# Performance work log

Hardware: AMD Instinct MI355X
Metric: run time of the kernel (lower is better)

## Reference

```python
import jax, jax.numpy as jnp
import numpy as np

B, D, L = 8, 512, 4096
NHEAD = 8
HEAD_DIM = D // NHEAD
TRUNC_STD = 0.02


def setup_inputs() -> dict:
    key = jax.random.key(0)
    ks = jax.random.split(key, 7)
    return {
        "x": jax.random.normal(ks[0], (B, D, L, 1), jnp.float32),
        "y": jax.random.normal(ks[1], (B, D, 1, 1), jnp.float32),
        "Wq": jax.random.normal(ks[2], (D, D), jnp.float32) * TRUNC_STD,
        "Wk": jax.random.normal(ks[3], (D, D), jnp.float32) * TRUNC_STD,
        "Wv": jax.random.normal(ks[4], (D, D), jnp.float32) * TRUNC_STD,
        "WO_ring": jax.random.normal(ks[5], (D, D), jnp.float32) * TRUNC_STD,
        "bO_ring": jnp.zeros((D,), jnp.float32),
        "WO_star": jax.random.normal(ks[6], (D, D), jnp.float32) * TRUNC_STD,
        "bO_star": jnp.zeros((D,), jnp.float32),
    }


def reference(x, y, Wq, Wk, Wv, WO_ring, bO_ring, WO_star, bO_star):
    Bx, Dx, Lx, _ = x.shape
    hd = Dx // NHEAD
    scale = 1.0 / np.sqrt(hd).astype(np.float32)

    # concat relay token on the sequence axis, project q/k/v over channels
    xy = jnp.concatenate([x, y], axis=2)[..., 0]            # [B, D, L+1]
    xy = jnp.transpose(xy, (0, 2, 1))                       # [B, L+1, D]
    q = jnp.transpose(xy @ Wq, (0, 2, 1))                   # [B, D, L+1]
    k = jnp.transpose(xy @ Wk, (0, 2, 1))
    v = jnp.transpose(xy @ Wv, (0, 2, 1))

    # ---- ring (local window-3 + relay) attention over the L node tokens ----
    qn = q[:, :, :Lx].reshape(Bx, NHEAD, hd, Lx)            # [B,n,h,L]
    kn, vn = k[:, :, :Lx], v[:, :, :Lx]                     # [B,D,L]
    kr, vr = k[:, :, Lx], v[:, :, Lx]                       # [B,D]

    def window3(t):
        # extract_patches SAME with size 3: slot w holds t[:, :, l-1+w], zero-padded
        tp = jnp.pad(t, ((0, 0), (0, 0), (1, 1)))
        tw = jnp.stack([tp[:, :, w:w + Lx] for w in range(3)], axis=2)  # [B,D,3,L]
        return tw.reshape(Bx, NHEAD, hd, 3, Lx)

    kr_b = jnp.broadcast_to(kr.reshape(Bx, NHEAD, hd, 1, 1), (Bx, NHEAD, hd, 1, Lx))
    vr_b = jnp.broadcast_to(vr.reshape(Bx, NHEAD, hd, 1, 1), (Bx, NHEAD, hd, 1, Lx))
    kw = jnp.concatenate([window3(kn), kr_b], axis=3)       # [B,n,h,4,L]
    vw = jnp.concatenate([window3(vn), vr_b], axis=3)

    scores = jnp.einsum('bnhl,bnhwl->bnwl', qn, kw) * scale  # [B,n,4,L]
    alphas = jax.nn.softmax(scores, axis=2)                  # softmax over window
    att = jnp.einsum('bnwl,bnhwl->bnhl', alphas, vw).reshape(Bx, Dx, Lx)
    nodes = jnp.einsum('bdl,de->bel', att, WO_ring) + bO_ring[None, :, None]
    nodes = nodes[..., None]                                 # [B, D, L, 1]

    # ---- star (relay) attention: relay query attends to all L+1 tokens ----
    qr = q[:, :, Lx].reshape(Bx, NHEAD, 1, hd)              # [B,n,1,h]
    ka = k.reshape(Bx, NHEAD, hd, Lx + 1)                   # [B,n,h,L+1]
    va = v.reshape(Bx, NHEAD, hd, Lx + 1)
    s = jnp.einsum('bnoh,bnhl->bnol', qr, ka) * scale       # [B,n,1,L+1]
    a = jax.nn.softmax(s, axis=-1)
    att_r = jnp.einsum('bnol,bnhl->bnoh', a, va).reshape(Bx, Dx)
    relay = (att_r @ WO_star + bO_star).reshape(Bx, Dx, 1, 1)

    return nodes, relay
```

## Files before the change

### kernel.cpp

```cpp
#include <hip/hip_runtime.h>

#define BB 8
#define DD 512
#define LL 4096
#define NH 8
#define HD 64
#define SCALE 0.125f
#define NCH2 128

typedef __attribute__((ext_vector_type(8))) short short8;
typedef __attribute__((ext_vector_type(4))) float f32x4;

static __device__ __forceinline__ float bf2f(unsigned short u) {
  union { float f; unsigned int i; } c; c.i = ((unsigned int)u) << 16; return c.f;
}
static __device__ __forceinline__ unsigned short f2bf(float f) {
  union { float f; unsigned int i; } c; c.f = f;
  unsigned int i = c.i;
  unsigned int r = (i + 0x7fffu + ((i >> 16) & 1u)) >> 16;
  return (unsigned short)r;
}

static __device__ __forceinline__ void gload_lds16(const void* g, void* l) {
  __builtin_amdgcn_global_load_lds(
      (const __attribute__((address_space(1))) void*)g,
      (__attribute__((address_space(3))) void*)l, 16, 0, 0);
}

static __device__ __forceinline__ float waveSum(float v) {
#pragma unroll
  for (int o = 32; o; o >>= 1) v += __shfl_down(v, o, 64);
  return v;
}
static __device__ __forceinline__ float grp8Sum(float v) {
  v += __shfl_xor(v, 1, 8);
  v += __shfl_xor(v, 2, 8);
  v += __shfl_xor(v, 4, 8);
  return v;
}
static __device__ __forceinline__ float waveAllMax(float v) {
#pragma unroll
  for (int o = 1; o < 64; o <<= 1) v = fmaxf(v, __shfl_xor(v, o, 64));
  return v;
}
static __device__ __forceinline__ float waveAllSum(float v) {
#pragma unroll
  for (int o = 1; o < 64; o <<= 1) v += __shfl_xor(v, o, 64);
  return v;
}

__global__ __launch_bounds__(256) void prep_w4(
    const float* __restrict__ w0, const float* __restrict__ w1,
    const float* __restrict__ w2, const float* __restrict__ w3,
    unsigned short* __restrict__ o0, unsigned short* __restrict__ o1,
    unsigned short* __restrict__ o2, unsigned short* __restrict__ o3) {
  const int s = blockIdx.z;
  const float* win = (s == 0) ? w0 : (s == 1) ? w1 : (s == 2) ? w2 : w3;
  unsigned short* wout = (s == 0) ? o0 : (s == 1) ? o1 : (s == 2) ? o2 : o3;
  const int d0 = blockIdx.y * 64;
  const int m0 = blockIdx.x * 64;
  __shared__ float t[64][65];
  const int tid = threadIdx.x;
  const int r = tid >> 4;
  const int c4 = (tid & 15) * 4;
#pragma unroll
  for (int p = 0; p < 4; p++) {
    const float4 v = *(const float4*)(win + (size_t)(d0 + p * 16 + r) * DD + m0 + c4);
    *(float4*)&t[p * 16 + r][c4] = v;
  }
  __syncthreads();
#pragma unroll
  for (int p = 0; p < 4; p++) {
    const int ll = p * 16 + r;
    ushort4 o;
    o.x = f2bf(t[c4 + 0][ll]);
    o.y = f2bf(t[c4 + 1][ll]);
    o.z = f2bf(t[c4 + 2][ll]);
    o.w = f2bf(t[c4 + 3][ll]);
    *(ushort4*)(wout + (size_t)(m0 + ll) * DD + d0 + c4) = o;
  }
}

__global__ __launch_bounds__(256) void prep_x(
    const float* __restrict__ x, unsigned short* __restrict__ xt) {
  const int b = blockIdx.z;
  const int e0 = blockIdx.y * 64;
  const int l0 = blockIdx.x * 64;
  __shared__ float t[64][65];
  const int tid = threadIdx.x;
  const int r = tid >> 4;
  const int c4 = (tid & 15) * 4;
  const float* xb = x + (size_t)b * DD * LL;
#pragma unroll
  for (int p = 0; p < 4; p++) {
    const float4 v = *(const float4*)(xb + (size_t)(e0 + p * 16 + r) * LL + l0 + c4);
    *(float4*)&t[p * 16 + r][c4] = v;
  }
  __syncthreads();
#pragma unroll
  for (int p = 0; p < 4; p++) {
    const int ll = p * 16 + r;
    ushort4 o;
    o.x = f2bf(t[c4 + 0][ll]);
    o.y = f2bf(t[c4 + 1][ll]);
    o.z = f2bf(t[c4 + 2][ll]);
    o.w = f2bf(t[c4 + 3][ll]);
    *(ushort4*)(xt + ((size_t)b * LL + l0 + ll) * DD + e0 + c4) = o;
  }
}

#define STAGEH(g, s)                                       \
  do {                                                     \
    gload_lds16((g) + sgoff, (s) + sloff);                 \
    gload_lds16((g) + sgoff + 32, (s) + sloff + 4096);     \
  } while (0)

#define READ_A(dst, base, ib)                                           \
  _Pragma("unroll") for (int i = 0; i < 4; i++) {                       \
    dst[i][0] = *(const short8*)((base) + ((ib) + i) * 512);            \
    dst[i][1] = *(const short8*)((base) + ((ib) + i) * 512 + 4096);     \
  }

#define READ_B(base, qn_)                                               \
  _Pragma("unroll") for (int j = 0; j < 2; j++) {                       \
    bb[j][0] = *(const short8*)((base) + (qn_) * 1024 + j * 512);       \
    bb[j][1] = *(const short8*)((base) + (qn_) * 1024 + j * 512 + 4096);\
  }

#define MFMA16(AF, IO, JO)                                                    \
  __builtin_amdgcn_s_setprio(1);                                              \
  _Pragma("unroll") for (int i = 0; i < 4; i++)                               \
  _Pragma("unroll") for (int j = 0; j < 2; j++) {                             \
    acc[(IO) + i][(JO) + j] = __builtin_amdgcn_mfma_f32_16x16x32_bf16(        \
        AF[i][0], bb[j][0], acc[(IO) + i][(JO) + j], 0, 0, 0);                \
    acc[(IO) + i][(JO) + j] = __builtin_amdgcn_mfma_f32_16x16x32_bf16(        \
        AF[i][1], bb[j][1], acc[(IO) + i][(JO) + j], 0, 0, 0);                \
  }                                                                           \
  __builtin_amdgcn_s_setprio(0);

#define PHASE_SYNC_PRE                                     \
  __builtin_amdgcn_s_barrier();                            \
  asm volatile("s_waitcnt lgkmcnt(0)" ::: "memory");       \
  __builtin_amdgcn_sched_barrier(0);

#define PHASE_SYNC_POST                                    \
  __builtin_amdgcn_sched_barrier(0);                       \
  __builtin_amdgcn_s_barrier();

__global__ __launch_bounds__(512, 2) void qkv_mfma_8ph(
    const unsigned short* __restrict__ Wt, const unsigned short* __restrict__ Xt,
    unsigned short* __restrict__ qn, unsigned short* __restrict__ kn,
    unsigned short* __restrict__ vn) {
  extern __shared__ __align__(16) unsigned short sm[];
  const int b = blockIdx.z;
  const int m0 = blockIdx.y * 256;
  const int n0 = blockIdx.x * 256;
  const int tid = threadIdx.x;
  const int lane = tid & 63, w = tid >> 6;
  const int wm = w >> 2, wn = w & 3;
  const int l15 = lane & 15, lh = lane >> 4;

  const unsigned short* Ag = Wt + (size_t)m0 * DD;
  const unsigned short* Bg = Xt + ((size_t)b * LL + n0) * DD;

  const int kswz = (lh << 3) ^ ((l15 & 8) << 1);
  const unsigned short* aB = sm + wm * 8192 + l15 * 32 + kswz;
  const unsigned short* bB = sm + 32768 + (wn >> 1) * 8192 + (wn & 1) * 2048 +
                             l15 * 32 + kswz;

  const int srow = (w << 4) + (lane >> 2);
  const size_t sgoff = (size_t)srow * DD + ((size_t)(((lane & 3) << 3) ^ ((srow & 8) << 1)));
  const int sloff = w * 512;

  f32x4 acc[8][4];
#pragma unroll
  for (int i = 0; i < 8; i++)
#pragma unroll
    for (int j = 0; j < 4; j++) acc[i][j] = (f32x4){0.f, 0.f, 0.f, 0.f};

  STAGEH(Ag, sm);
  STAGEH(Ag + 128 * DD, sm + 8192);
  STAGEH(Bg, sm + 32768);
  STAGEH(Bg + 128 * DD, sm + 32768 + 8192);
  STAGEH(Ag + 64, sm + 16384);
  STAGEH(Ag + 128 * DD + 64, sm + 16384 + 8192);
  asm volatile("s_waitcnt vmcnt(4)" ::: "memory");
  __builtin_amdgcn_s_barrier();

  short8 a0[4][2], a1[4][2], bb[2][2];
  for (int u = 0; u < 8; ++u) {
    const int slot = u & 1;
    const unsigned short* aS = aB + slot * 16384;
    const unsigned short* bS = bB + slot * 16384;
    const unsigned short* An = Ag + (u + 2) * 64;
    const unsigned short* Bn = Bg + (u + 1) * 64;
    unsigned short* sAd = sm + slot * 16384;
    unsigned short* sBd = sm + 32768 + (slot ^ 1) * 16384;

    READ_A(a0, aS, 0);
    READ_B(bS, 0);
    if (u < 7) STAGEH(Bn, sBd);
    PHASE_SYNC_PRE
    MFMA16(a0, 0, 0)
    PHASE_SYNC_POST
    READ_A(a1, aS, 4);
    if (u < 7) STAGEH(Bn + 128 * DD, sBd + 8192);
    PHASE_SYNC_PRE
    MFMA16(a1, 4, 0)
    PHASE_SYNC_POST
    READ_B(bS, 1);
    if (u < 6) STAGEH(An, sAd);
    PHASE_SYNC_PRE
    MFMA16(a0, 0, 2)
    PHASE_SYNC_POST
    if (u < 6) STAGEH(An + 128 * DD, sAd + 8192);
    __builtin_amdgcn_s_barrier();
    asm volatile("s_waitcnt lgkmcnt(0)" ::: "memory");
    __builtin_amdgcn_sched_barrier(0);
    MFMA16(a1, 4, 2)
    __builtin_amdgcn_sched_barrier(0);
    if (u < 6) {
      asm volatile("s_waitcnt vmcnt(4)" ::: "memory");
    } else if (u == 6) {
      asm volatile("s_waitcnt vmcnt(0)" ::: "memory");
    }
    __builtin_amdgcn_s_barrier();
  }

  __syncthreads();
#pragma unroll
  for (int i = 0; i < 8; i++)
#pragma unroll
    for (int j = 0; j < 4; j++) {
      const int dloc = wm * 128 + i * 16 + lh * 4;
      const int lloc = wn * 64 + j * 16 + l15;
      ushort4 pk;
      pk.x = f2bf(acc[i][j][0]);
      pk.y = f2bf(acc[i][j][1]);
      pk.z = f2bf(acc[i][j][2]);
      pk.w = f2bf(acc[i][j][3]);
      *(ushort4*)((char*)sm + ((lloc * 512 + dloc * 2) ^ ((lloc & 7) << 4))) = pk;
    }
  __syncthreads();
  const int sector = m0 >> 9;
  unsigned short* outp = ((sector == 0) ? qn : (sector == 1) ? kn : vn) +
                         (size_t)b * LL * DD + (m0 & 511);
#pragma unroll
  for (int it = 0; it < 16; it++) {
    const int flat = it * 8192 + tid * 16;
    const int lloc = flat >> 9;
    const int off = flat & 511;
    const short8 vdat =
        *(const short8*)((const char*)sm + lloc * 512 + (off ^ ((lloc & 7) << 4)));
    *(short8*)(outp + (size_t)(n0 + lloc) * DD + (off >> 1)) = vdat;
  }
}

__global__ __launch_bounds__(256) void nodes_mfma(
    const unsigned short* __restrict__ Wt, const unsigned short* __restrict__ At,
    const float* __restrict__ bo, float* __restrict__ out) {
  const int wgid = blockIdx.x + 32 * (blockIdx.y + 4 * blockIdx.z);
  const int swz = (wgid & 7) * 128 + (wgid >> 3);
  const int b = swz >> 7;
  const int rem = swz & 127;
  const int n0 = (rem >> 2) * 128;
  const int m0 = (rem & 3) * 128;
  __shared__ short As[128 * 32];
  __shared__ short Bs[128 * 32];
  const int tid = threadIdx.x;
  const int lane = tid & 63, w = tid >> 6;
  const int wm = w & 1, wn = w >> 1;

  const unsigned short* Ag = Wt + (size_t)m0 * DD;
  const unsigned short* Bg = At + ((size_t)b * LL + n0) * DD;
  const int srow = lane >> 2;
  const int scol = (lane & 3) * 8;

  f32x4 acc[4][4];
#pragma unroll
  for (int i = 0; i < 4; i++)
#pragma unroll
    for (int j = 0; j < 4; j++) acc[i][j] = (f32x4){0.f, 0.f, 0.f, 0.f};

  for (int k0 = 0; k0 < DD; k0 += 32) {
    __syncthreads();
#pragma unroll
    for (int p = 0; p < 2; p++) {
      const int c = w * 2 + p;
      gload_lds16(Ag + (size_t)(c * 16 + srow) * DD + k0 + scol, (short*)As + c * 16 * 32);
      gload_lds16(Bg + (size_t)(c * 16 + srow) * DD + k0 + scol, (short*)Bs + c * 16 * 32);
    }
    __syncthreads();
    short8 af[4], bfr[4];
#pragma unroll
    for (int i = 0; i < 4; i++)
      af[i] = *(const short8*)&As[(wm * 64 + i * 16 + (lane & 15)) * 32 + (lane >> 4) * 8];
#pragma unroll
    for (int j = 0; j < 4; j++)
      bfr[j] = *(const short8*)&Bs[(wn * 64 + j * 16 + (lane & 15)) * 32 + (lane >> 4) * 8];
#pragma unroll
    for (int i = 0; i < 4; i++)
#pragma unroll
      for (int j = 0; j < 4; j++)
        acc[i][j] = __builtin_amdgcn_mfma_f32_16x16x32_bf16(af[i], bfr[j], acc[i][j], 0, 0, 0);
  }

  float* outp = out + (size_t)b * DD * LL;
  const int ebase = m0 + wm * 64;
  const int col0 = n0 + wn * 64 + (lane & 15);
#pragma unroll
  for (int i = 0; i < 4; i++) {
    const int e0 = ebase + i * 16 + (lane >> 4) * 4;
#pragma unroll
    for (int j = 0; j < 4; j++) {
      const int cc = col0 + j * 16;
#pragma unroll
      for (int r = 0; r < 4; r++)
        outp[(size_t)(e0 + r) * LL + cc] = acc[i][j][r] + bo[e0 + r];
    }
  }
}

__global__ __launch_bounds__(256) void relay_qkv(
    const float* __restrict__ y, const float* __restrict__ Wq,
    const float* __restrict__ Wk, const float* __restrict__ Wv,
    float* __restrict__ qr, float* __restrict__ kr, float* __restrict__ vr) {
  const int b = blockIdx.y;
  const int d0 = blockIdx.x * 64;
  const int tid = threadIdx.x;
  const int dl = tid & 63, eg = tid >> 6;
  __shared__ float ys[DD];
  __shared__ float r3[3][4][64];
  for (int i = tid; i < DD; i += 256) ys[i] = y[b * DD + i];
  __syncthreads();
  float aq = 0.f, ak = 0.f, av = 0.f;
  const int e0 = eg * 128;
  for (int e = e0; e < e0 + 128; e++) {
    const float yv = ys[e];
    aq = fmaf(yv, Wq[(size_t)e * DD + d0 + dl], aq);
    ak = fmaf(yv, Wk[(size_t)e * DD + d0 + dl], ak);
    av = fmaf(yv, Wv[(size_t)e * DD + d0 + dl], av);
  }
  r3[0][eg][dl] = aq;
  r3[1][eg][dl] = ak;
  r3[2][eg][dl] = av;
  __syncthreads();
  if (tid < 192) {
    const int m = tid >> 6, d = tid & 63;
    const float s = r3[m][0][d] + r3[m][1][d] + r3[m][2][d] + r3[m][3][d];
    float* dst = (m == 0) ? qr : (m == 1) ? kr : vr;
    dst[b * DD + d0 + d] = s;
  }
}

__global__ __launch_bounds__(256) void local_attn_f(
    const unsigned short* __restrict__ qn, const unsigned short* __restrict__ kn,
    const unsigned short* __restrict__ vn, const float* __restrict__ kr,
    const float* __restrict__ vr, const float* __restrict__ qrg,
    unsigned short* __restrict__ att_t, float* __restrict__ part) {
  const int b = blockIdx.z, n = blockIdx.y;
  const int tid = threadIdx.x;
  const int li = tid >> 3, dl = tid & 7;
  const int l0 = blockIdx.x * 32;
  const int l = l0 + li;
  __shared__ float krs[HD], vrs[HD], qrs[HD];
  __shared__ __align__(16) char ksb[34 * 128];
  __shared__ __align__(16) char vsb[34 * 128];
  __shared__ float sv2[32];
  __shared__ float os[32][68];
  const int rb = b * DD + n * HD;
  if (tid < HD) {
    krs[tid] = kr[rb + tid];
    vrs[tid] = vr[rb + tid];
    qrs[tid] = qrg[rb + tid];
  }

  {
    const int s1 = tid >> 3;
    const int gl1 = min(max(l0 - 1 + s1, 0), LL - 1);
    const size_t gb1 = ((size_t)b * LL + gl1) * DD + n * HD + dl * 8;
    const int so1 = s1 * 128 + dl * 16;
    *(short8*)(ksb + so1) = *(const short8*)(kn + gb1);
    *(short8*)(vsb + so1) = *(const short8*)(vn + gb1);
    if (tid < 16) {
      const int s2 = 32 + (tid >> 3);
      const int gl2 = min(l0 - 1 + s2, LL - 1);
      const size_t gb2 = ((size_t)b * LL + gl2) * DD + n * HD + dl * 8;
      const int so2 = s2 * 128 + dl * 16;
      *(short8*)(ksb + so2) = *(const short8*)(kn + gb2);
      *(short8*)(vsb + so2) = *(const short8*)(vn + gb2);
    }
  }
  __syncthreads();

  const size_t rowbase = ((size_t)b * LL + l) * DD + n * HD + dl * 8;
  const bool has_m = (l > 0), has_p = (l < LL - 1);
  const int lo = dl * 16;

  const short8 q8 = *(const short8*)(qn + rowbase);
  const short8 km8 = *(const short8*)(ksb + (li + 0) * 128 + lo);
  const short8 k08 = *(const short8*)(ksb + (li + 1) * 128 + lo);
  const short8 kp8 = *(const short8*)(ksb + (li + 2) * 128 + lo);

  float s0 = 0.f, s1 = 0.f, s2 = 0.f, s3 = 0.f;
  float qf[8];
#pragma unroll
  for (int j = 0; j < 8; j++) {
    qf[j] = bf2f((unsigned short)q8[j]);
    s0 = fmaf(qf[j], bf2f((unsigned short)km8[j]), s0);
    s1 = fmaf(qf[j], bf2f((unsigned short)k08[j]), s1);
    s2 = fmaf(qf[j], bf2f((unsigned short)kp8[j]), s2);
    s3 = fmaf(qf[j], krs[dl * 8 + j], s3);
  }
  s0 = grp8Sum(s0) * SCALE;
  s1 = grp8Sum(s1) * SCALE;
  s2 = grp8Sum(s2) * SCALE;
  s3 = grp8Sum(s3) * SCALE;
  if (!has_m) s0 = 0.f;
  if (!has_p) s2 = 0.f;
  const float m = fmaxf(fmaxf(s0, s1), fmaxf(s2, s3));
  const float e0 = __expf(s0 - m), e1 = __expf(s1 - m);
  const float e2 = __expf(s2 - m), e3 = __expf(s3 - m);
  const float inv = 1.f / (e0 + e1 + e2 + e3);
  const float a0 = has_m ? e0 * inv : 0.f;
  const float a1 = e1 * inv;
  const float a2 = has_p ? e2 * inv : 0.f;
  const float a3 = e3 * inv;

  const short8 vm8 = *(const short8*)(vsb + (li + 0) * 128 + lo);
  const short8 v08 = *(const short8*)(vsb + (li + 1) * 128 + lo);
  const short8 vp8 = *(const short8*)(vsb + (li + 2) * 128 + lo);
  short8 o8;
#pragma unroll
  for (int j = 0; j < 8; j++) {
    float o = a0 * bf2f((unsigned short)vm8[j]) + a1 * bf2f((unsigned short)v08[j]) +
              a2 * bf2f((unsigned short)vp8[j]) + a3 * vrs[dl * 8 + j];
    o8[j] = (short)f2bf(o);
  }
  *(short8*)(att_t + rowbase) = o8;

  {
    const short8 kc = *(const short8*)(ksb + (li + 1) * 128 + lo);
    float p = 0.f;
#pragma unroll
    for (int j = 0; j < 8; j++) p = fmaf(qrs[dl * 8 + j], bf2f((unsigned short)kc[j]), p);
    p = grp8Sum(p);
    if (dl == 0) sv2[li] = p * SCALE;
  }
  __syncthreads();
  const int lane = tid & 63;
  const float sval = sv2[lane & 31];
  const float m2 = waveAllMax(sval);
  const float sum2 = waveAllSum((lane < 32) ? __expf(sval - m2) : 0.f);
  const float pp = __expf(sv2[li] - m2);
  {
    const short8 vc = *(const short8*)(vsb + (li + 1) * 128 + lo);
#pragma unroll
    for (int j = 0; j < 8; j++) os[li][dl * 8 + j] = pp * bf2f((unsigned short)vc[j]);
  }
  __syncthreads();
  float* po = part + (((size_t)b * NH + n) * NCH2 + blockIdx.x) * 68;
  if (tid < HD) {
    float t = 0.f;
#pragma unroll 8
    for (int g = 0; g < 32; g++) t += os[g][tid];
    po[tid] = t;
  }
  if (tid == 64) { po[64] = m2; po[65] = sum2; }
}

__global__ __launch_bounds__(64) void relay_attn_combine(
    const float* __restrict__ qr, const float* __restrict__ krr,
    const float* __restrict__ vrr, const float* __restrict__ part,
    float* __restrict__ attr) {
  const int n = blockIdx.x, b = blockIdx.y;
  const int h = threadIdx.x;
  const int rb = b * DD + n * HD;
  float t = qr[rb + h] * krr[rb + h];
  t = waveSum(t);
  const float s_r = __shfl(t, 0, 64) * SCALE;
  const float* po = part + (((size_t)b * NH + n) * NCH2) * 68;
  float M = s_r;
#pragma unroll 8
  for (int c = 0; c < NCH2; c++) M = fmaxf(M, po[c * 68 + 64]);
  float S = __expf(s_r - M);
  float o = S * vrr[rb + h];
#pragma unroll 4
  for (int c = 0; c < NCH2; c++) {
    const float e = __expf(po[c * 68 + 64] - M);
    S = fmaf(po[c * 68 + 65], e, S);
    o = fmaf(po[c * 68 + h], e, o);
  }
  attr[rb + h] = o / S;
}

__global__ __launch_bounds__(256) void relay_proj(
    const float* __restrict__ attr, const float* __restrict__ Wstar,
    const float* __restrict__ bstar, float* __restrict__ out) {
  const int b = blockIdx.y;
  const int e0 = blockIdx.x * 64;
  const int tid = threadIdx.x;
  const int el = tid & 63, dg = tid >> 6;
  __shared__ float as[DD];
  __shared__ float r[4][64];
  for (int i = tid; i < DD; i += 256) as[i] = attr[b * DD + i];
  __syncthreads();
  float acc = 0.f;
  const int d0 = dg * 128;
  for (int d = d0; d < d0 + 128; d++)
    acc = fmaf(as[d], Wstar[(size_t)d * DD + e0 + el], acc);
  r[dg][el] = acc;
  __syncthreads();
  if (tid < 64)
    out[(size_t)BB * DD * LL + b * DD + e0 + tid] =
        r[0][tid] + r[1][tid] + r[2][tid] + r[3][tid] + bstar[e0 + tid];
}

extern "C" void kernel_launch(void* const* d_in, const int* in_sizes, int n_in,
                              void* d_out, int out_size, void* d_ws, size_t ws_size,
                              hipStream_t stream) {
  const float* x   = (const float*)d_in[0];
  const float* y   = (const float*)d_in[1];
  const float* Wq  = (const float*)d_in[2];
  const float* Wk  = (const float*)d_in[3];
  const float* Wv  = (const float*)d_in[4];
  const float* WOr = (const float*)d_in[5];
  const float* bOr = (const float*)d_in[6];
  const float* WOs = (const float*)d_in[7];
  const float* bOs = (const float*)d_in[8];
  float* out = (float*)d_out;

  char* ws = (char*)d_ws;
  const size_t SZ = (size_t)BB * DD * LL * sizeof(unsigned short);
  unsigned short* qn  = (unsigned short*)(ws);
  unsigned short* kn  = (unsigned short*)(ws + SZ);
  unsigned short* vn  = (unsigned short*)(ws + 2 * SZ);
  unsigned short* xt  = (unsigned short*)(ws + 3 * SZ);
  unsigned short* att_t = xt;
  unsigned short* Wallt = (unsigned short*)(ws + 4 * SZ);
  unsigned short* WOrt  = (unsigned short*)(ws + 4 * SZ + 1536 * 512 * 2);
  float* qr   = (float*)(ws + 4 * SZ + 2048 * 512 * 2);
  float* kr   = qr + BB * DD;
  float* vr   = kr + BB * DD;
  float* attr = vr + BB * DD;
  float* part = attr + BB * DD;

  static int smaxset = 0;
  if (!smaxset) {
    (void)hipFuncSetAttribute((const void*)qkv_mfma_8ph,
                              hipFuncAttributeMaxDynamicSharedMemorySize, 131072);
    smaxset = 1;
  }

  prep_w4<<<dim3(8, 8, 4), 256, 0, stream>>>(
      Wq, Wk, Wv, WOr,
      Wallt, Wallt + (size_t)512 * 512, Wallt + (size_t)1024 * 512, WOrt);
  prep_x<<<dim3(64, 8, BB), 256, 0, stream>>>(x, xt);

  qkv_mfma_8ph<<<dim3(16, 6, BB), 512, 131072, stream>>>(Wallt, xt, qn, kn, vn);
  relay_qkv<<<dim3(8, BB), 256, 0, stream>>>(y, Wq, Wk, Wv, qr, kr, vr);
  local_attn_f<<<dim3(LL / 32, NH, BB), 256, 0, stream>>>(qn, kn, vn, kr, vr, qr,
                                                          att_t, part);
  nodes_mfma<<<dim3(32, 4, BB), 256, 0, stream>>>(WOrt, att_t, bOr, out);
  relay_attn_combine<<<dim3(NH, BB), 64, 0, stream>>>(qr, kr, vr, part, attr);
  relay_proj<<<dim3(8, BB), 256, 0, stream>>>(attr, WOs, bOs, out);
}
```

Before: 294.9 us.

## Reuse 8-phase 256x256 GEMM core for output projection and fuse small launches

Factors the pipelined 8-phase MFMA GEMM body into a macro and uses it for the ring output projection, replacing the simpler 128x128 single-buffered kernel with 256x256 tiles and double-buffered LDS staging. It also merges the weight and x conversion kernels into one launch and folds the relay softmax combine into the relay projection kernel. This cuts launch count and aims for better MFMA utilisation in the nodes GEMM. The cost is only 256 workgroups for that GEMM, which may underfill the GPU, and the relay combine is now recomputed by each of the 8 column blocks per batch.

```diff
diff --git a/kernel.cpp b/kernel.cpp
--- a/kernel.cpp
+++ b/kernel.cpp
@@ -49,63 +49,62 @@
   return v;
 }
 
-__global__ __launch_bounds__(256) void prep_w4(
+__global__ __launch_bounds__(256) void prep_all(
+    const float* __restrict__ x, unsigned short* __restrict__ xt,
     const float* __restrict__ w0, const float* __restrict__ w1,
     const float* __restrict__ w2, const float* __restrict__ w3,
     unsigned short* __restrict__ o0, unsigned short* __restrict__ o1,
     unsigned short* __restrict__ o2, unsigned short* __restrict__ o3) {
-  const int s = blockIdx.z;
-  const float* win = (s == 0) ? w0 : (s == 1) ? w1 : (s == 2) ? w2 : w3;
-  unsigned short* wout = (s == 0) ? o0 : (s == 1) ? o1 : (s == 2) ? o2 : o3;
-  const int d0 = blockIdx.y * 64;
-  const int m0 = blockIdx.x * 64;
   __shared__ float t[64][65];
   const int tid = threadIdx.x;
   const int r = tid >> 4;
   const int c4 = (tid & 15) * 4;
-#pragma unroll
-  for (int p = 0; p < 4; p++) {
-    const float4 v = *(const float4*)(win + (size_t)(d0 + p * 16 + r) * DD + m0 + c4);
-    *(float4*)&t[p * 16 + r][c4] = v;
-  }
-  __syncthreads();
-#pragma unroll
-  for (int p = 0; p < 4; p++) {
-    const int ll = p * 16 + r;
-    ushort4 o;
-    o.x = f2bf(t[c4 + 0][ll]);
-    o.y = f2bf(t[c4 + 1][ll]);
-    o.z = f2bf(t[c4 + 2][ll]);
-    o.w = f2bf(t[c4 + 3][ll]);
-    *(ushort4*)(wout + (size_t)(m0 + ll) * DD + d0 + c4) = o;
-  }
-}
-
-__global__ __launch_bounds__(256) void prep_x(
-    const float* __restrict__ x, unsigned short* __restrict__ xt) {
-  const int b = blockIdx.z;
-  const int e0 = blockIdx.y * 64;
-  const int l0 = blockIdx.x * 64;
-  __shared__ float t[64][65];
-  const int tid = threadIdx.x;
-  const int r = tid >> 4;
-  const int c4 = (tid & 15) * 4;
-  const float* xb = x + (size_t)b * DD * LL;
-#pragma unroll
-  for (int p = 0; p < 4; p++) {
-    const float4 v = *(const float4*)(xb + (size_t)(e0 + p * 16 + r) * LL + l0 + c4);
-    *(float4*)&t[p * 16 + r][c4] = v;
-  }
-  __syncthreads();
-#pragma unroll
-  for (int p = 0; p < 4; p++) {
-    const int ll = p * 16 + r;
-    ushort4 o;
-    o.x = f2bf(t[c4 + 0][ll]);
-    o.y = f2bf(t[c4 + 1][ll]);
-    o.z = f2bf(t[c4 + 2][ll]);
-    o.w = f2bf(t[c4 + 3][ll]);
-    *(ushort4*)(xt + ((size_t)b * LL + l0 + ll) * DD + e0 + c4) = o;
+  if (blockIdx.z < BB) {
+    const int b = blockIdx.z;
+    const int e0 = blockIdx.y * 64;
+    const int l0 = blockIdx.x * 64;
+    const float* xb = x + (size_t)b * DD * LL;
+#pragma unroll
+    for (int p = 0; p < 4; p++) {
+      const float4 v = *(const float4*)(xb + (size_t)(e0 + p * 16 + r) * LL + l0 + c4);
+      *(float4*)&t[p * 16 + r][c4] = v;
+    }
+    __syncthreads();
+#pragma unroll
+    for (int p = 0; p < 4; p++) {
+      const int ll = p * 16 + r;
+      ushort4 o;
+      o.x = f2bf(t[c4 + 0][ll]);
+      o.y = f2bf(t[c4 + 1][ll]);
+      o.z = f2bf(t[c4 + 2][ll]);
+      o.w = f2bf(t[c4 + 3][ll]);
+      *(ushort4*)(xt + ((size_t)b * LL + l0 + ll) * DD + e0 + c4) = o;
+    }
+  } else {
+    const int wid = blockIdx.x + 64 * blockIdx.y;
+    if (wid >= 256) return;
+    const int s = wid >> 6;
+    const int tb = wid & 63;
+    const int m0 = (tb & 7) * 64;
+    const int d0 = (tb >> 3) * 64;
+    const float* win = (s == 0) ? w0 : (s == 1) ? w1 : (s == 2) ? w2 : w3;
+    unsigned short* wout = (s == 0) ? o0 : (s == 1) ? o1 : (s == 2) ? o2 : o3;
+#pragma unroll
+    for (int p = 0; p < 4; p++) {
+      const float4 v = *(const float4*)(win + (size_t)(d0 + p * 16 + r) * DD + m0 + c4);
+      *(float4*)&t[p * 16 + r][c4] = v;
+    }
+    __syncthreads();
+#pragma unroll
+    for (int p = 0; p < 4; p++) {
+      const int ll = p * 16 + r;
+      ushort4 o;
+      o.x = f2bf(t[c4 + 0][ll]);
+      o.y = f2bf(t[c4 + 1][ll]);
+      o.z = f2bf(t[c4 + 2][ll]);
+      o.w = f2bf(t[c4 + 3][ll]);
+      *(ushort4*)(wout + (size_t)(m0 + ll) * DD + d0 + c4) = o;
+    }
   }
 }
 
@@ -147,6 +146,69 @@
   __builtin_amdgcn_sched_barrier(0);                       \
   __builtin_amdgcn_s_barrier();
 
+#define GEMM_8PH_CORE                                                         \
+  const int lane = tid & 63, w = tid >> 6;                                    \
+  const int wm = w >> 2, wn = w & 3;                                          \
+  const int l15 = lane & 15, lh = lane >> 4;                                  \
+  const int kswz = (lh << 3) ^ ((l15 & 8) << 1);                              \
+  const unsigned short* aB = sm + wm * 8192 + l15 * 32 + kswz;                \
+  const unsigned short* bB = sm + 32768 + (wn >> 1) * 8192 +                  \
+                             (wn & 1) * 2048 + l15 * 32 + kswz;               \
+  const int srow = (w << 4) + (lane >> 2);                                    \
+  const size_t sgoff = (size_t)srow * DD +                                    \
+      ((size_t)(((lane & 3) << 3) ^ ((srow & 8) << 1)));                      \
+  const int sloff = w * 512;                                                  \
+  f32x4 acc[8][4];                                                            \
+  _Pragma("unroll") for (int i = 0; i < 8; i++)                               \
+  _Pragma("unroll") for (int j = 0; j < 4; j++)                               \
+      acc[i][j] = (f32x4){0.f, 0.f, 0.f, 0.f};                                \
+  STAGEH(Ag, sm);                                                             \
+  STAGEH(Ag + 128 * DD, sm + 8192);                                           \
+  STAGEH(Bg, sm + 32768);                                                     \
+  STAGEH(Bg + 128 * DD, sm + 32768 + 8192);                                   \
+  STAGEH(Ag + 64, sm + 16384);                                                \
+  STAGEH(Ag + 128 * DD + 64, sm + 16384 + 8192);                              \
+  asm volatile("s_waitcnt vmcnt(4)" ::: "memory");                            \
+  __builtin_amdgcn_s_barrier();                                               \
+  short8 a0[4][2], a1[4][2], bb[2][2];                                        \
+  for (int u = 0; u < 8; ++u) {                                               \
+    const int slot = u & 1;                                                   \
+    const unsigned short* aS = aB + slot * 16384;                             \
+    const unsigned short* bS = bB + slot * 16384;                             \
+    const unsigned short* An = Ag + (u + 2) * 64;                             \
+    const unsigned short* Bn = Bg + (u + 1) * 64;                             \
+    unsigned short* sAd = sm + slot * 16384;                                  \
+    unsigned short* sBd = sm + 32768 + (slot ^ 1) * 16384;                    \
+    READ_A(a0, aS, 0);                                                        \
+    READ_B(bS, 0);                                                            \
+    if (u < 7) STAGEH(Bn, sBd);                                               \
+    PHASE_SYNC_PRE                                                            \
+    MFMA16(a0, 0, 0)                                                          \
+    PHASE_SYNC_POST                                                           \
+    READ_A(a1, aS, 4);                                                        \
+    if (u < 7) STAGEH(Bn + 128 * DD, sBd + 8192);                             \
+    PHASE_SYNC_PRE                                                            \
+    MFMA16(a1, 4, 0)                                                          \
+    PHASE_SYNC_POST                                                           \
+    READ_B(bS, 1);                                                            \
+    if (u < 6) STAGEH(An, sAd);                                               \
+    PHASE_SYNC_PRE                                                            \
+    MFMA16(a0, 0, 2)                                                          \
+    PHASE_SYNC_POST                                                           \
+    if (u < 6) STAGEH(An + 128 * DD, sAd + 8192);                             \
+    __builtin_amdgcn_s_barrier();                                             \
+    asm volatile("s_waitcnt lgkmcnt(0)" ::: "memory");                        \
+    __builtin_amdgcn_sched_barrier(0);                                        \
+    MFMA16(a1, 4, 2)                                                          \
+    __builtin_amdgcn_sched_barrier(0);                                        \
+    if (u < 6) {                                                              \
+      asm volatile("s_waitcnt vmcnt(4)" ::: "memory");                        \
+    } else if (u == 6) {                                                      \
+      asm volatile("s_waitcnt vmcnt(0)" ::: "memory");                        \
+    }                                                                         \
+    __builtin_amdgcn_s_barrier();                                             \
+  }
+
 __global__ __launch_bounds__(512, 2) void qkv_mfma_8ph(
     const unsigned short* __restrict__ Wt, const unsigned short* __restrict__ Xt,
     unsigned short* __restrict__ qn, unsigned short* __restrict__ kn,
@@ -156,76 +218,10 @@
   const int m0 = blockIdx.y * 256;
   const int n0 = blockIdx.x * 256;
   const int tid = threadIdx.x;
-  const int lane = tid & 63, w = tid >> 6;
-  const int wm = w >> 2, wn = w & 3;
-  const int l15 = lane & 15, lh = lane >> 4;
-
   const unsigned short* Ag = Wt + (size_t)m0 * DD;
   const unsigned short* Bg = Xt + ((size_t)b * LL + n0) * DD;
 
-  const int kswz = (lh << 3) ^ ((l15 & 8) << 1);
-  const unsigned short* aB = sm + wm * 8192 + l15 * 32 + kswz;
-  const unsigned short* bB = sm + 32768 + (wn >> 1) * 8192 + (wn & 1) * 2048 +
-                             l15 * 32 + kswz;
-
-  const int srow = (w << 4) + (lane >> 2);
-  const size_t sgoff = (size_t)srow * DD + ((size_t)(((lane & 3) << 3) ^ ((srow & 8) << 1)));
-  const int sloff = w * 512;
-
-  f32x4 acc[8][4];
-#pragma unroll
-  for (int i = 0; i < 8; i++)
-#pragma unroll
-    for (int j = 0; j < 4; j++) acc[i][j] = (f32x4){0.f, 0.f, 0.f, 0.f};
-
-  STAGEH(Ag, sm);
-  STAGEH(Ag + 128 * DD, sm + 8192);
-  STAGEH(Bg, sm + 32768);
-  STAGEH(Bg + 128 * DD, sm + 32768 + 8192);
-  STAGEH(Ag + 64, sm + 16384);
-  STAGEH(Ag + 128 * DD + 64, sm + 16384 + 8192);
-  asm volatile("s_waitcnt vmcnt(4)" ::: "memory");
-  __builtin_amdgcn_s_barrier();
-
-  short8 a0[4][2], a1[4][2], bb[2][2];
-  for (int u = 0; u < 8; ++u) {
-    const int slot = u & 1;
-    const unsigned short* aS = aB + slot * 16384;
-    const unsigned short* bS = bB + slot * 16384;
-    const unsigned short* An = Ag + (u + 2) * 64;
-    const unsigned short* Bn = Bg + (u + 1) * 64;
-    unsigned short* sAd = sm + slot * 16384;
-    unsigned short* sBd = sm + 32768 + (slot ^ 1) * 16384;
-
-    READ_A(a0, aS, 0);
-    READ_B(bS, 0);
-    if (u < 7) STAGEH(Bn, sBd);
-    PHASE_SYNC_PRE
-    MFMA16(a0, 0, 0)
-    PHASE_SYNC_POST
-    READ_A(a1, aS, 4);
-    if (u < 7) STAGEH(Bn + 128 * DD, sBd + 8192);
-    PHASE_SYNC_PRE
-    MFMA16(a1, 4, 0)
-    PHASE_SYNC_POST
-    READ_B(bS, 1);
-    if (u < 6) STAGEH(An, sAd);
-    PHASE_SYNC_PRE
-    MFMA16(a0, 0, 2)
-    PHASE_SYNC_POST
-    if (u < 6) STAGEH(An + 128 * DD, sAd + 8192);
-    __builtin_amdgcn_s_barrier();
-    asm volatile("s_waitcnt lgkmcnt(0)" ::: "memory");
-    __builtin_amdgcn_sched_barrier(0);
-    MFMA16(a1, 4, 2)
-    __builtin_amdgcn_sched_barrier(0);
-    if (u < 6) {
-      asm volatile("s_waitcnt vmcnt(4)" ::: "memory");
-    } else if (u == 6) {
-      asm volatile("s_waitcnt vmcnt(0)" ::: "memory");
-    }
-    __builtin_amdgcn_s_barrier();
-  }
+  GEMM_8PH_CORE
 
   __syncthreads();
 #pragma unroll
@@ -256,67 +252,31 @@
   }
 }
 
-__global__ __launch_bounds__(256) void nodes_mfma(
+__global__ __launch_bounds__(512, 2) void nodes_mfma_8ph(
     const unsigned short* __restrict__ Wt, const unsigned short* __restrict__ At,
     const float* __restrict__ bo, float* __restrict__ out) {
-  const int wgid = blockIdx.x + 32 * (blockIdx.y + 4 * blockIdx.z);
-  const int swz = (wgid & 7) * 128 + (wgid >> 3);
-  const int b = swz >> 7;
-  const int rem = swz & 127;
-  const int n0 = (rem >> 2) * 128;
-  const int m0 = (rem & 3) * 128;
-  __shared__ short As[128 * 32];
-  __shared__ short Bs[128 * 32];
+  extern __shared__ __align__(16) unsigned short sm[];
+  const int b = blockIdx.z;
+  const int m0 = blockIdx.y * 256;
+  const int n0 = blockIdx.x * 256;
   const int tid = threadIdx.x;
-  const int lane = tid & 63, w = tid >> 6;
-  const int wm = w & 1, wn = w >> 1;
-
   const unsigned short* Ag = Wt + (size_t)m0 * DD;
   const unsigned short* Bg = At + ((size_t)b * LL + n0) * DD;
-  const int srow = lane >> 2;
-  const int scol = (lane & 3) * 8;
-
-  f32x4 acc[4][4];
-#pragma unroll
-  for (int i = 0; i < 4; i++)
-#pragma unroll
-    for (int j = 0; j < 4; j++) acc[i][j] = (f32x4){0.f, 0.f, 0.f, 0.f};
-
-  for (int k0 = 0; k0 < DD; k0 += 32) {
-    __syncthreads();
-#pragma unroll
-    for (int p = 0; p < 2; p++) {
-      const int c = w * 2 + p;
-      gload_lds16(Ag + (size_t)(c * 16 + srow) * DD + k0 + scol, (short*)As + c * 16 * 32);
-      gload_lds16(Bg + (size_t)(c * 16 + srow) * DD + k0 + scol, (short*)Bs + c * 16 * 32);
-    }
-    __syncthreads();
-    short8 af[4], bfr[4];
-#pragma unroll
-    for (int i = 0; i < 4; i++)
-      af[i] = *(const short8*)&As[(wm * 64 + i * 16 + (lane & 15)) * 32 + (lane >> 4) * 8];
-#pragma unroll
-    for (int j = 0; j < 4; j++)
-      bfr[j] = *(const short8*)&Bs[(wn * 64 + j * 16 + (lane & 15)) * 32 + (lane >> 4) * 8];
-#pragma unroll
-    for (int i = 0; i < 4; i++)
-#pragma unroll
-      for (int j = 0; j < 4; j++)
-        acc[i][j] = __builtin_amdgcn_mfma_f32_16x16x32_bf16(af[i], bfr[j], acc[i][j], 0, 0, 0);
-  }
+
+  GEMM_8PH_CORE
 
   float* outp = out + (size_t)b * DD * LL;
-  const int ebase = m0 + wm * 64;
-  const int col0 = n0 + wn * 64 + (lane & 15);
-#pragma unroll
-  for (int i = 0; i < 4; i++) {
-    const int e0 = ebase + i * 16 + (lane >> 4) * 4;
-#pragma unroll
-    for (int j = 0; j < 4; j++) {
-      const int cc = col0 + j * 16;
-#pragma unroll
-      for (int r = 0; r < 4; r++)
-        outp[(size_t)(e0 + r) * LL + cc] = acc[i][j][r] + bo[e0 + r];
+  const int ebase = m0 + wm * 128;
+  const int col0 = n0 + wn * 64 + l15;
+#pragma unroll
+  for (int i = 0; i < 8; i++) {
+    const int e0r = ebase + i * 16 + lh * 4;
+#pragma unroll
+    for (int r = 0; r < 4; r++) {
+      const float bv = bo[e0r + r];
+      float* rowp = outp + (size_t)(e0r + r) * LL + col0;
+#pragma unroll
+      for (int j = 0; j < 4; j++) rowp[j * 16] = acc[i][j][r] + bv;
     }
   }
 }
@@ -469,42 +429,40 @@
   if (tid == 64) { po[64] = m2; po[65] = sum2; }
 }
 
-__global__ __launch_bounds__(64) void relay_attn_combine(
+__global__ __launch_bounds__(256) void relay_proj_f(
     const float* __restrict__ qr, const float* __restrict__ krr,
     const float* __restrict__ vrr, const float* __restrict__ part,
-    float* __restrict__ attr) {
-  const int n = blockIdx.x, b = blockIdx.y;
-  const int h = threadIdx.x;
-  const int rb = b * DD + n * HD;
-  float t = qr[rb + h] * krr[rb + h];
-  t = waveSum(t);
-  const float s_r = __shfl(t, 0, 64) * SCALE;
-  const float* po = part + (((size_t)b * NH + n) * NCH2) * 68;
-  float M = s_r;
-#pragma unroll 8
-  for (int c = 0; c < NCH2; c++) M = fmaxf(M, po[c * 68 + 64]);
-  float S = __expf(s_r - M);
-  float o = S * vrr[rb + h];
-#pragma unroll 4
-  for (int c = 0; c < NCH2; c++) {
-    const float e = __expf(po[c * 68 + 64] - M);
-    S = fmaf(po[c * 68 + 65], e, S);
-    o = fmaf(po[c * 68 + h], e, o);
-  }
-  attr[rb + h] = o / S;
-}
-
-__global__ __launch_bounds__(256) void relay_proj(
-    const float* __restrict__ attr, const float* __restrict__ Wstar,
-    const float* __restrict__ bstar, float* __restrict__ out) {
+    const float* __restrict__ Wstar, const float* __restrict__ bstar,
+    float* __restrict__ out) {
   const int b = blockIdx.y;
   const int e0 = blockIdx.x * 64;
   const int tid = threadIdx.x;
-  const int el = tid & 63, dg = tid >> 6;
+  const int lane = tid & 63, w = tid >> 6;
   __shared__ float as[DD];
   __shared__ float r[4][64];
-  for (int i = tid; i < DD; i += 256) as[i] = attr[b * DD + i];
-  __syncthreads();
+#pragma unroll
+  for (int pass = 0; pass < 2; ++pass) {
+    const int n = w + pass * 4;
+    const int rb = b * DD + n * HD;
+    float t = qr[rb + lane] * krr[rb + lane];
+    t = waveSum(t);
+    const float s_r = __shfl(t, 0, 64) * SCALE;
+    const float* po = part + (((size_t)b * NH + n) * NCH2) * 68;
+    float M = s_r;
+#pragma unroll 8
+    for (int c = 0; c < NCH2; c++) M = fmaxf(M, po[c * 68 + 64]);
+    float S = __expf(s_r - M);
+    float o = S * vrr[rb + lane];
+#pragma unroll 4
+    for (int c = 0; c < NCH2; c++) {
+      const float e = __expf(po[c * 68 + 64] - M);
+      S = fmaf(po[c * 68 + 65], e, S);
+      o = fmaf(po[c * 68 + lane], e, o);
+    }
+    as[n * HD + lane] = o / S;
+  }
+  __syncthreads();
+  const int el = tid & 63, dg = tid >> 6;
   float acc = 0.f;
   const int d0 = dg * 128;
   for (int d = d0; d < d0 + 128; d++)
@@ -542,26 +500,25 @@
   float* qr   = (float*)(ws + 4 * SZ + 2048 * 512 * 2);
   float* kr   = qr + BB * DD;
   float* vr   = kr + BB * DD;
-  float* attr = vr + BB * DD;
-  float* part = attr + BB * DD;
+  float* part = vr + BB * DD;
 
   static int smaxset = 0;
   if (!smaxset) {
     (void)hipFuncSetAttribute((const void*)qkv_mfma_8ph,
                               hipFuncAttributeMaxDynamicSharedMemorySize, 131072);
+    (void)hipFuncSetAttribute((const void*)nodes_mfma_8ph,
+                              hipFuncAttributeMaxDynamicSharedMemorySize, 131072);
     smaxset = 1;
   }
 
-  prep_w4<<<dim3(8, 8, 4), 256, 0, stream>>>(
-      Wq, Wk, Wv, WOr,
+  prep_all<<<dim3(64, 8, BB + 1), 256, 0, stream>>>(
+      x, xt, Wq, Wk, Wv, WOr,
       Wallt, Wallt + (size_t)512 * 512, Wallt + (size_t)1024 * 512, WOrt);
-  prep_x<<<dim3(64, 8, BB), 256, 0, stream>>>(x, xt);
 
   qkv_mfma_8ph<<<dim3(16, 6, BB), 512, 131072, stream>>>(Wallt, xt, qn, kn, vn);
   relay_qkv<<<dim3(8, BB), 256, 0, stream>>>(y, Wq, Wk, Wv, qr, kr, vr);
   local_attn_f<<<dim3(LL / 32, NH, BB), 256, 0, stream>>>(qn, kn, vn, kr, vr, qr,
                                                           att_t, part);
-  nodes_mfma<<<dim3(32, 4, BB), 256, 0, stream>>>(WOrt, att_t, bOr, out);
-  relay_attn_combine<<<dim3(NH, BB), 64, 0, stream>>>(qr, kr, vr, part, attr);
-  relay_proj<<<dim3(8, BB), 256, 0, stream>>>(attr, WOs, bOs, out);
-}
+  nodes_mfma_8ph<<<dim3(16, 2, BB), 512, 131072, stream>>>(WOrt, att_t, bOr, out);
+  relay_proj_f<<<dim3(8, BB), 256, 0, stream>>>(qr, kr, vr, part, WOs, bOs, out);
+}
```

Result: slower. 323.7 us (+9.8%).
